# Kernel optimization log

Measured on AMD Instinct MI355X. Metric: run time of the kernel, lower is better.

## Reference

```python
import jax, jax.numpy as jnp
import numpy as np

N_SPATIAL = 65160
N_SPHERE = 2883
N_EDGES = 131072
D = 256             # latent_size
EDGE_IN_FIRST = 3 + 2 * D   # raw 3-dim displacements + sender + receiver = 515
EDGE_IN_REST = 3 * D        # after step 1 edges are D-dim = 768
NODE_IN = 2 * D
N_STEPS = 3


def _layernorm(x, g, b, eps=1e-5):
    m = jnp.mean(x, axis=-1, keepdims=True)
    v = jnp.var(x, axis=-1, keepdims=True)
    return (x - m) * jax.lax.rsqrt(v + eps) * g + b


def _mlp(x, W1, b1, g, o, W2, b2):
    # Linear -> relu -> LayerNorm -> Linear (matches hk.Sequential)
    h = jax.nn.relu(x @ W1 + b1)
    return _layernorm(h, g, o) @ W2 + b2


def setup_inputs() -> dict:
    key = jax.random.key(0)
    ks = jax.random.split(key, 12)

    def glorot(k, shape):
        return jax.random.normal(k, shape, jnp.float32) / np.sqrt(shape[0]).astype(np.float32)

    nodes = jax.random.normal(ks[0], (N_SPATIAL + N_SPHERE, D), jnp.float32)
    edges = jax.random.normal(ks[1], (N_EDGES, 3), jnp.float32)
    senders = jax.random.randint(ks[2], (N_EDGES,), 0, N_SPATIAL)
    # receivers index into the sphere portion of the concatenated node array
    receivers = jax.random.randint(ks[3], (N_EDGES,), 0, N_SPHERE) + N_SPATIAL
    return {
        "nodes": nodes,
        "edges": edges,
        "senders": senders,
        "receivers": receivers,
        "We1a": glorot(ks[4], (EDGE_IN_FIRST, D)),
        "We1b": glorot(ks[5], (EDGE_IN_REST, D)),
        "be1": jnp.zeros((D,), jnp.float32),
        "ge": jnp.ones((D,), jnp.float32),
        "oe": jnp.zeros((D,), jnp.float32),
        "We2": glorot(ks[6], (D, D)),
        "be2": jnp.zeros((D,), jnp.float32),
        "Wn1": glorot(ks[7], (NODE_IN, D)),
        "bn1": jnp.zeros((D,), jnp.float32),
        "gn": jnp.ones((D,), jnp.float32),
        "on": jnp.zeros((D,), jnp.float32),
        "Wn2": glorot(ks[8], (D, D)),
        "bn2": jnp.zeros((D,), jnp.float32),
        "n_spatial": N_SPATIAL,
        "n_sphere": N_SPHERE,
    }


def reference(nodes, edges, senders, receivers,
              We1a, We1b, be1, ge, oe, We2, be2,
              Wn1, bn1, gn, on, Wn2, bn2,
              n_spatial, n_sphere):
    recv_ids = receivers - n_spatial  # local sphere indices in [0, n_sphere)
    for step in range(N_STEPS):
        s = nodes[senders]                                   # [E, D]
        r = nodes[receivers]                                 # [E, D]
        edge_in = jnp.concatenate([edges, s, r], axis=1)     # [E, 3+2D] or [E, 3D]
        W1 = We1a if step == 0 else We1b
        edges = _mlp(edge_in, W1, be1, ge, oe, We2, be2)     # [E, D]
        messages = jax.ops.segment_sum(edges, recv_ids, num_segments=n_sphere)  # [S, D]
        sphere = nodes[n_spatial:]                           # [S, D]
        node_in = jnp.concatenate([sphere, messages], axis=1)
        updated = _mlp(node_in, Wn1, bn1, gn, on, Wn2, bn2)  # [S, D]
        nodes = jnp.concatenate([nodes[:n_spatial], updated], axis=0)
    return nodes[n_spatial:]
```

## Files before the change

### kernel.cpp

```cpp
#include <hip/hip_runtime.h>
#include <hip/hip_bf16.h>
#include <cstdint>
#include <cstddef>

#define N_SPATIAL_C 65160
#define N_SPHERE_C  2883
#define N_EDGES_C   131072

typedef short bf16x8 __attribute__((ext_vector_type(8)));
typedef float f32x4  __attribute__((ext_vector_type(4)));

__device__ inline float bf2f(ushort u) {
    union { uint u; float f; } c; c.u = ((uint)u) << 16; return c.f;
}
__device__ inline ushort f2bf(float f) {
    __hip_bfloat16 h = __float2bfloat16(f);
    union { __hip_bfloat16 h; ushort u; } c; c.h = h; return c.u;
}

#define VMWAIT8()  asm volatile("s_waitcnt vmcnt(8)" ::: "memory")
#define VMWAIT0()  asm volatile("s_waitcnt vmcnt(0)" ::: "memory")
#define LGKM0()    asm volatile("s_waitcnt lgkmcnt(0)" ::: "memory")
#define SBAR()     do { __builtin_amdgcn_sched_barrier(0); \
                        __builtin_amdgcn_s_barrier(); \
                        __builtin_amdgcn_sched_barrier(0); } while (0)

template<int EPI, int KI, int NBUF, typename OutT>
__global__ __launch_bounds__(256, 2) void mfma_gemm(
    const ushort* __restrict__ A, const ushort* __restrict__ Bt,
    OutT* __restrict__ C, int M, int lda, int ldc,
    const float* __restrict__ bias,
    const float* __restrict__ g, const float* __restrict__ o,
    const ushort* __restrict__ P, const int* __restrict__ senders,
    const float* __restrict__ Rf, const int* __restrict__ receivers,
    const int* __restrict__ cntv, const float* __restrict__ bxv)
{
    constexpr int CHR = KI / 8;
    __shared__ __align__(16) ushort lds[NBUF][64 * KI];

    const int nt = (M + 63) >> 6;
    if ((int)blockIdx.x >= nt) return;
    const int G    = gridDim.x;
    const int t    = threadIdx.x;
    const int w    = t >> 6;
    const int lane = t & 63;
    const int lo   = lane & 15, hi = lane >> 4, sw = lo & 7;
    const int bn   = w * 64;
    const int rl   = t >> 4, q = t & 15, c0 = q * 16;

    auto STAGE = [&](int buf, int tileIdx) {
#pragma unroll
        for (int i = 0; i < (64 * CHR) / 256; ++i) {
            int ci = i * 256 + t;
            int r  = ci / CHR;
            int cs = ci % CHR;
            int cg = cs ^ (r & 7);
            int rg = tileIdx * 64 + r; if (rg >= M) rg = M - 1;
            const ushort* gp = A + (size_t)rg * lda + cg * 8;
            const ushort* lp = &lds[buf][(size_t)(i * 256 + w * 64) * 8];
            __builtin_amdgcn_global_load_lds(
                (const __attribute__((address_space(1))) unsigned int*)gp,
                (__attribute__((address_space(3))) unsigned int*)lp, 16, 0, 0);
        }
    };

    bf16x8 breg[(NBUF == 2) ? 8 : 1][4];
    if constexpr (NBUF == 2) {
#pragma unroll
        for (int ks = 0; ks < 8; ++ks)
#pragma unroll
            for (int ct = 0; ct < 4; ++ct)
                breg[ks][ct] = *reinterpret_cast<const bf16x8*>(
                    Bt + (size_t)(bn + ct * 16 + lo) * KI + ks * 32 + hi * 8);
        STAGE(0, blockIdx.x);
    }

    int cur = 0;
    for (int tt = blockIdx.x; tt < nt; tt += G) {
        if constexpr (NBUF == 1) {
            STAGE(0, tt);
            VMWAIT0();
        } else {
            int tn = tt + G;
            if (tn < nt) { STAGE(cur ^ 1, tn); VMWAIT8(); }
            else         { VMWAIT0(); }
        }
        SBAR();

        const ushort* At = lds[cur];
        f32x4 acc[4][4];
#pragma unroll
        for (int rt = 0; rt < 4; ++rt)
#pragma unroll
            for (int ct = 0; ct < 4; ++ct)
#pragma unroll
                for (int j = 0; j < 4; ++j) acc[rt][ct][j] = 0.f;

#pragma unroll
        for (int ks = 0; ks < KI / 32; ++ks) {
            bf16x8 av[4], bv[4];
#pragma unroll
            for (int rt = 0; rt < 4; ++rt) {
                int row = rt * 16 + lo;
                av[rt] = *reinterpret_cast<const bf16x8*>(
                    At + ((size_t)row * CHR + ((ks * 4 + hi) ^ sw)) * 8);
            }
            if constexpr (NBUF == 2) {
#pragma unroll
                for (int ct = 0; ct < 4; ++ct) bv[ct] = breg[ks][ct];
            } else {
#pragma unroll
                for (int ct = 0; ct < 4; ++ct)
                    bv[ct] = *reinterpret_cast<const bf16x8*>(
                        Bt + (size_t)(bn + ct * 16 + lo) * KI + ks * 32 + hi * 8);
            }
#pragma unroll
            for (int rt = 0; rt < 4; ++rt)
#pragma unroll
                for (int ct = 0; ct < 4; ++ct)
                    acc[rt][ct] = __builtin_amdgcn_mfma_f32_16x16x32_bf16(
                        av[rt], bv[ct], acc[rt][ct], 0, 0, 0);
        }

        float* xbuf = (float*)lds[cur];
#pragma unroll
        for (int ph = 0; ph < 4; ++ph) {
            LGKM0(); SBAR();
#pragma unroll
            for (int ct = 0; ct < 4; ++ct)
#pragma unroll
                for (int reg = 0; reg < 4; ++reg)
                    xbuf[(size_t)(hi * 4 + reg) * 260 + (bn + ct * 16 + lo)] =
                        acc[ph][ct][reg];
            LGKM0(); SBAR();

            int rowg = tt * 64 + ph * 16 + rl;
            bool ok  = rowg < M;
            int rowc = ok ? rowg : M - 1;

            float x[16];
#pragma unroll
            for (int jj = 0; jj < 4; ++jj) {
                f32x4 v = *reinterpret_cast<const f32x4*>(
                    xbuf + (size_t)rl * 260 + c0 + jj * 4);
                x[jj*4+0] = v[0]; x[jj*4+1] = v[1];
                x[jj*4+2] = v[2]; x[jj*4+3] = v[3];
            }
            if (bias) {
#pragma unroll
                for (int jj = 0; jj < 4; ++jj) {
                    f32x4 v = *reinterpret_cast<const f32x4*>(bias + c0 + jj * 4);
                    x[jj*4+0] += v[0]; x[jj*4+1] += v[1];
                    x[jj*4+2] += v[2]; x[jj*4+3] += v[3];
                }
            }
            if (EPI == 1 && cntv) {
                float cf = (float)cntv[rowc];
#pragma unroll
                for (int jj = 0; jj < 4; ++jj) {
                    f32x4 v = *reinterpret_cast<const f32x4*>(bxv + c0 + jj * 4);
                    x[jj*4+0] += cf * v[0]; x[jj*4+1] += cf * v[1];
                    x[jj*4+2] += cf * v[2]; x[jj*4+3] += cf * v[3];
                }
            }
            if (EPI == 2) {
                int sIdx = senders[rowc];
                int rIdx = receivers[rowc] - N_SPATIAL_C;
                bf16x8 p0 = *reinterpret_cast<const bf16x8*>(P + (size_t)sIdx * 256 + c0);
                bf16x8 p1 = *reinterpret_cast<const bf16x8*>(P + (size_t)sIdx * 256 + c0 + 8);
#pragma unroll
                for (int j = 0; j < 8; ++j) {
                    x[j]     += bf2f((ushort)p0[j]);
                    x[8 + j] += bf2f((ushort)p1[j]);
                }
#pragma unroll
                for (int jj = 0; jj < 4; ++jj) {
                    f32x4 v = *reinterpret_cast<const f32x4*>(
                        Rf + (size_t)rIdx * 256 + c0 + jj * 4);
                    x[jj*4+0] += v[0]; x[jj*4+1] += v[1];
                    x[jj*4+2] += v[2]; x[jj*4+3] += v[3];
                }
            }
            if (EPI >= 1) {
#pragma unroll
                for (int j = 0; j < 16; ++j) x[j] = fmaxf(x[j], 0.f);
                float s1 = 0.f, s2 = 0.f;
#pragma unroll
                for (int j = 0; j < 16; ++j) { s1 += x[j]; s2 += x[j] * x[j]; }
#pragma unroll
                for (int m = 1; m < 16; m <<= 1) {
                    s1 += __shfl_xor(s1, m);
                    s2 += __shfl_xor(s2, m);
                }
                float mean = s1 * (1.f / 256.f);
                float var  = s2 * (1.f / 256.f) - mean * mean;
                float rstd = rsqrtf(var + 1e-5f);
#pragma unroll
                for (int jj = 0; jj < 4; ++jj) {
                    f32x4 gv = *reinterpret_cast<const f32x4*>(g + c0 + jj * 4);
                    f32x4 ov = *reinterpret_cast<const f32x4*>(o + c0 + jj * 4);
#pragma unroll
                    for (int e = 0; e < 4; ++e)
                        x[jj*4+e] = (x[jj*4+e] - mean) * rstd * gv[e] + ov[e];
                }
            }
            if (ok) {
                if constexpr (sizeof(OutT) == 2) {
                    bf16x8 s0, s1v;
#pragma unroll
                    for (int j = 0; j < 8; ++j) {
                        s0[j]  = (short)f2bf(x[j]);
                        s1v[j] = (short)f2bf(x[8 + j]);
                    }
                    ushort* Cp = (ushort*)C + (size_t)rowg * ldc + c0;
                    *reinterpret_cast<bf16x8*>(Cp)     = s0;
                    *reinterpret_cast<bf16x8*>(Cp + 8) = s1v;
                } else {
                    float* Cp = (float*)C + (size_t)rowg * ldc + c0;
#pragma unroll
                    for (int jj = 0; jj < 4; ++jj) {
                        f32x4 v;
                        v[0]=x[jj*4+0]; v[1]=x[jj*4+1];
                        v[2]=x[jj*4+2]; v[3]=x[jj*4+3];
                        *reinterpret_cast<f32x4*>(Cp + jj * 4) = v;
                    }
                }
            }
        }
        LGKM0(); SBAR();
        if constexpr (NBUF == 2) cur ^= 1;
    }
}

__global__ __launch_bounds__(256) void fuse0(
    const float* __restrict__ edges3, const float* __restrict__ Ae,
    const ushort* __restrict__ P, const int* __restrict__ senders,
    const float* __restrict__ Rf, const int* __restrict__ receivers,
    const float* __restrict__ be1, const float* __restrict__ g,
    const float* __restrict__ o, ushort* __restrict__ H)
{
    int row  = blockIdx.x * 4 + (threadIdx.x >> 6);
    int lane = threadIdx.x & 63;
    int c = lane * 4;

    float e0 = edges3[(size_t)row * 3 + 0];
    float e1 = edges3[(size_t)row * 3 + 1];
    float e2 = edges3[(size_t)row * 3 + 2];
    int s = senders[row];
    int r = receivers[row] - N_SPATIAL_C;
    ushort4 pv = *reinterpret_cast<const ushort4*>(P + (size_t)s * 256 + c);
    float4  rv = *reinterpret_cast<const float4*>(Rf + (size_t)r * 256 + c);

    float pw[4] = {bf2f(pv.x), bf2f(pv.y), bf2f(pv.z), bf2f(pv.w)};
    float rw[4] = {rv.x, rv.y, rv.z, rv.w};
    float x[4];
#pragma unroll
    for (int j = 0; j < 4; ++j) {
        x[j] = e0 * Ae[c + j] + e1 * Ae[256 + c + j] + e2 * Ae[512 + c + j]
             + be1[c + j] + pw[j] + rw[j];
        x[j] = fmaxf(x[j], 0.f);
    }
    float s1 = x[0] + x[1] + x[2] + x[3];
    float s2 = x[0]*x[0] + x[1]*x[1] + x[2]*x[2] + x[3]*x[3];
#pragma unroll
    for (int m = 32; m > 0; m >>= 1) { s1 += __shfl_xor(s1, m); s2 += __shfl_xor(s2, m); }
    float mean = s1 * (1.f / 256.f);
    float var  = s2 * (1.f / 256.f) - mean * mean;
    float rstd = rsqrtf(var + 1e-5f);
#pragma unroll
    for (int j = 0; j < 4; ++j) {
        float y = (x[j] - mean) * rstd * g[c + j] + o[c + j];
        H[(size_t)row * 256 + c + j] = f2bf(y);
    }
}

__global__ void count_k(const int* __restrict__ receivers, int* __restrict__ cnt)
{
    int e = blockIdx.x * 256 + threadIdx.x;
    if (e < N_EDGES_C) atomicAdd(&cnt[receivers[e] - N_SPATIAL_C], 1);
}

__global__ void scan_k(const int* __restrict__ cnt, int* __restrict__ row_start)
{
    __shared__ int sums[257];
    const int CH = 12;
    int t = threadIdx.x;
    int local = 0;
    for (int i = 0; i < CH; ++i) {
        int idx = t * CH + i;
        if (idx < N_SPHERE_C) local += cnt[idx];
    }
    sums[t] = local;
    __syncthreads();
    if (t == 0) {
        int run = 0;
        for (int i = 0; i < 256; ++i) { int v = sums[i]; sums[i] = run; run += v; }
        sums[256] = run;
    }
    __syncthreads();
    int base = sums[t];
    for (int i = 0; i < CH; ++i) {
        int idx = t * CH + i;
        if (idx < N_SPHERE_C) { row_start[idx] = base; base += cnt[idx]; }
    }
    if (t == 0) row_start[N_SPHERE_C] = sums[256];
}

__global__ void fill_k(const int* __restrict__ receivers, const int* __restrict__ row_start,
                       int* __restrict__ cursor, int* __restrict__ csr)
{
    int e = blockIdx.x * 256 + threadIdx.x;
    if (e < N_EDGES_C) {
        int rid = receivers[e] - N_SPATIAL_C;
        int pos = atomicAdd(&cursor[rid], 1);
        csr[row_start[rid] + pos] = e;
    }
}

__global__ __launch_bounds__(256) void seg_gather(
    const ushort* __restrict__ H, const int* __restrict__ row_start,
    const int* __restrict__ csr, ushort* __restrict__ S, int ldS)
{
    __shared__ float red[3][64][4];
    int n = blockIdx.x;
    int sub = threadIdx.x >> 6, l = threadIdx.x & 63, c = l * 4;
    int beg = row_start[n], end = row_start[n + 1];
    float a0 = 0.f, a1 = 0.f, a2 = 0.f, a3 = 0.f;
    for (int i = beg + sub; i < end; i += 4) {
        int e = csr[i];
        ushort4 v = *reinterpret_cast<const ushort4*>(H + (size_t)e * 256 + c);
        a0 += bf2f(v.x); a1 += bf2f(v.y); a2 += bf2f(v.z); a3 += bf2f(v.w);
    }
    if (sub) { red[sub-1][l][0]=a0; red[sub-1][l][1]=a1; red[sub-1][l][2]=a2; red[sub-1][l][3]=a3; }
    __syncthreads();
    if (sub == 0) {
#pragma unroll
        for (int s_ = 0; s_ < 3; ++s_) {
            a0 += red[s_][l][0]; a1 += red[s_][l][1];
            a2 += red[s_][l][2]; a3 += red[s_][l][3];
        }
        ushort4 u; u.x = f2bf(a0); u.y = f2bf(a1); u.z = f2bf(a2); u.w = f2bf(a3);
        *reinterpret_cast<ushort4*>(S + (size_t)n * ldS + c) = u;
    }
}

__global__ __launch_bounds__(256) void wprod_kernel(
    const float* __restrict__ We2, const float* __restrict__ Bsrc,
    ushort* __restrict__ Wt, int ldd, int koff)
{
    __shared__ float colB[256];
    int j = blockIdx.x, k = threadIdx.x;
    colB[k] = Bsrc[(size_t)k * 256 + j];
    __syncthreads();
    const float* wrow = We2 + (size_t)k * 256;
    float acc = 0.f;
    for (int t = 0; t < 256; ++t) acc += wrow[t] * colB[t];
    Wt[(size_t)j * ldd + koff + k] = f2bf(acc);
}

__global__ void bvecprod_kernel(const float* __restrict__ base, const float* __restrict__ bvec,
                                const float* __restrict__ W, float* __restrict__ bout)
{
    int j = threadIdx.x;
    float acc = base ? base[j] : 0.f;
    for (int k = 0; k < 256; ++k) acc += bvec[k] * W[(size_t)k * 256 + j];
    bout[j] = acc;
}

__global__ void tcast2(const float* __restrict__ W, ushort* __restrict__ Wt, int ldd)
{
    __shared__ float tbuf[16][17];
    int k0 = blockIdx.x * 16, n0 = blockIdx.y * 16;
    int tx = threadIdx.x, ty = threadIdx.y;
    tbuf[ty][tx] = W[(size_t)(k0 + ty) * 256 + n0 + tx];
    __syncthreads();
    Wt[(size_t)(n0 + ty) * ldd + k0 + tx] = f2bf(tbuf[tx][ty]);
}

__global__ void cast_f32_bf16(const float* __restrict__ src, ushort* __restrict__ dst, int n4)
{
    int i = blockIdx.x * 256 + threadIdx.x;
    if (i < n4) {
        float4 v = *reinterpret_cast<const float4*>(src + (size_t)i * 4);
        ushort4 u;
        u.x = f2bf(v.x); u.y = f2bf(v.y); u.z = f2bf(v.z); u.w = f2bf(v.w);
        *reinterpret_cast<ushort4*>(dst + (size_t)i * 4) = u;
    }
}

__global__ void cast_sphere(const float* __restrict__ nodes, ushort* __restrict__ node_in)
{
    int n = blockIdx.x, d = threadIdx.x;
    node_in[(size_t)n * 512 + d] =
        f2bf(nodes[(size_t)(N_SPATIAL_C + n) * 256 + d]);
}

extern "C" void kernel_launch(void* const* d_in, const int* in_sizes, int n_in,
                              void* d_out, int out_size, void* d_ws, size_t ws_size,
                              hipStream_t stream)
{
    const float* nodes     = (const float*)d_in[0];
    const float* edges3    = (const float*)d_in[1];
    const int*   senders   = (const int*)d_in[2];
    const int*   receivers = (const int*)d_in[3];
    const float* We1a      = (const float*)d_in[4];
    const float* We1b      = (const float*)d_in[5];
    const float* be1       = (const float*)d_in[6];
    const float* ge        = (const float*)d_in[7];
    const float* oe        = (const float*)d_in[8];
    const float* We2       = (const float*)d_in[9];
    const float* be2       = (const float*)d_in[10];
    const float* Wn1       = (const float*)d_in[11];
    const float* bn1       = (const float*)d_in[12];
    const float* gn        = (const float*)d_in[13];
    const float* on_       = (const float*)d_in[14];
    const float* Wn2       = (const float*)d_in[15];
    const float* bn2       = (const float*)d_in[16];

    const float* Ae  = We1a;
    const float* As_ = We1a + 3 * 256;
    const float* Ar  = We1a + 259 * 256;
    const float* Be  = We1b;
    const float* Bs_ = We1b + 256 * 256;
    const float* Br  = We1b + 512 * 256;
    const float* Wn1bot = Wn1 + 256 * 256;

    char* ws = (char*)d_ws;
    size_t off = 0;
    auto alloc = [&](size_t b) -> char* {
        char* p = ws + off;
        off += (b + 255) & ~(size_t)255;
        return p;
    };
    ushort* H          = (ushort*)alloc((size_t)N_EDGES_C * 256 * 2);
    ushort* Pb         = (ushort*)alloc((size_t)N_SPATIAL_C * 256 * 2);
    ushort* nodes_bf   = (ushort*)alloc((size_t)N_SPATIAL_C * 256 * 2);
    float*  Rf         = (float*)alloc((size_t)N_SPHERE_C * 256 * 4);
    ushort* node_in_bf = (ushort*)alloc((size_t)N_SPHERE_C * 512 * 2);
    ushort* nH         = (ushort*)alloc((size_t)N_SPHERE_C * 256 * 2);
    ushort* Ast  = (ushort*)alloc(256 * 256 * 2);
    ushort* Art  = (ushort*)alloc(256 * 256 * 2);
    ushort* Bst  = (ushort*)alloc(256 * 256 * 2);
    ushort* Brt  = (ushort*)alloc(256 * 256 * 2);
    ushort* Wn2t = (ushort*)alloc(256 * 256 * 2);
    ushort* Wft  = (ushort*)alloc(256 * 256 * 2);
    ushort* Bnt  = (ushort*)alloc(256 * 512 * 2);
    float*  bfc  = (float*)alloc(256 * 4);
    float*  bxv  = (float*)alloc(256 * 4);
    int* cnt       = (int*)alloc(N_SPHERE_C * 4);
    int* cursor    = (int*)alloc(N_SPHERE_C * 4);
    int* row_start = (int*)alloc((N_SPHERE_C + 1) * 4);
    int* csr       = (int*)alloc((size_t)N_EDGES_C * 4);

    hipMemsetAsync(cnt, 0, N_SPHERE_C * 4, stream);
    hipMemsetAsync(cursor, 0, N_SPHERE_C * 4, stream);
    count_k<<<(N_EDGES_C + 255) / 256, 256, 0, stream>>>(receivers, cnt);
    scan_k<<<1, 256, 0, stream>>>(cnt, row_start);
    fill_k<<<(N_EDGES_C + 255) / 256, 256, 0, stream>>>(receivers, row_start, cursor, csr);

    dim3 tb(16, 16);
    tcast2<<<dim3(16, 16), tb, 0, stream>>>(As_, Ast, 256);
    tcast2<<<dim3(16, 16), tb, 0, stream>>>(Ar,  Art, 256);
    tcast2<<<dim3(16, 16), tb, 0, stream>>>(Bs_, Bst, 256);
    tcast2<<<dim3(16, 16), tb, 0, stream>>>(Br,  Brt, 256);
    tcast2<<<dim3(16, 16), tb, 0, stream>>>(Wn2, Wn2t, 256);
    tcast2<<<dim3(16, 16), tb, 0, stream>>>(Wn1, Bnt, 512);
    wprod_kernel<<<256, 256, 0, stream>>>(We2, Be, Wft, 256, 0);
    wprod_kernel<<<256, 256, 0, stream>>>(We2, Wn1bot, Bnt, 512, 256);
    bvecprod_kernel<<<1, 256, 0, stream>>>(be1, be2, Be, bfc);
    bvecprod_kernel<<<1, 256, 0, stream>>>(nullptr, be2, Wn1bot, bxv);

    cast_f32_bf16<<<(N_SPATIAL_C * 64 + 255) / 256, 256, 0, stream>>>(
        nodes, nodes_bf, N_SPATIAL_C * 64);
    cast_sphere<<<N_SPHERE_C, 256, 0, stream>>>(nodes, node_in_bf);

    const int GBIG = 512;
    const int GS = (N_SPHERE_C + 63) / 64;

    const float* nul = nullptr;

    mfma_gemm<0, 256, 2, ushort><<<GBIG, 256, 0, stream>>>(
        nodes_bf, Ast, Pb, N_SPATIAL_C, 256, 256,
        nul, nul, nul, nullptr, nullptr, nul, nullptr, nullptr, nul);

    for (int step = 0; step < 3; ++step) {
        mfma_gemm<0, 256, 2, float><<<GS, 256, 0, stream>>>(
            node_in_bf, step == 0 ? Art : Brt, Rf, N_SPHERE_C, 512, 256,
            nul, nul, nul, nullptr, nullptr, nul, nullptr, nullptr, nul);

        if (step == 0) {
            fuse0<<<N_EDGES_C / 4, 256, 0, stream>>>(
                edges3, Ae, Pb, senders, Rf, receivers, be1, ge, oe, H);
            mfma_gemm<0, 256, 2, ushort><<<GBIG, 256, 0, stream>>>(
                nodes_bf, Bst, Pb, N_SPATIAL_C, 256, 256,
                nul, nul, nul, nullptr, nullptr, nul, nullptr, nullptr, nul);
        } else {
            mfma_gemm<2, 256, 2, ushort><<<GBIG, 256, 0, stream>>>(
                H, Wft, H, N_EDGES_C, 256, 256,
                bfc, ge, oe, Pb, senders, Rf, receivers, nullptr, nul);
        }

        seg_gather<<<N_SPHERE_C, 256, 0, stream>>>(H, row_start, csr,
                                                   node_in_bf + 256, 512);

        mfma_gemm<1, 512, 1, ushort><<<GS, 256, 0, stream>>>(
            node_in_bf, Bnt, nH, N_SPHERE_C, 512, 256,
            bn1, gn, on_, nullptr, nullptr, nul, nullptr, cnt, bxv);

        if (step < 2) {
            mfma_gemm<0, 256, 2, ushort><<<GS, 256, 0, stream>>>(
                nH, Wn2t, node_in_bf, N_SPHERE_C, 256, 512,
                bn2, nul, nul, nullptr, nullptr, nul, nullptr, nullptr, nul);
        } else {
            mfma_gemm<0, 256, 2, float><<<GS, 256, 0, stream>>>(
                nH, Wn2t, (float*)d_out, N_SPHERE_C, 256, 256,
                bn2, nul, nul, nullptr, nullptr, nul, nullptr, nullptr, nul);
        }
    }
}
```

Before: 665.9 us.

## Replace LDS-staged persistent GEMM with direct-load register GEMM and register epilogue

Rewrites the MFMA GEMM kernel. It drops the persistent grid with double-buffered LDS staging through global_load_lds and swizzling. Each block now handles one 64-row tile, and A and B fragments are read straight from global memory into registers. The operand order is swapped so each lane holds a row's columns, which lets the bias, gather-add, ReLU and LayerNorm epilogue run in registers with only a small LDS cross-wave reduction, instead of transposing through LDS. This removes LDS traffic and barriers and raises the occupancy target, at the cost of uncoalesced, unreused global A and B loads with no prefetch overlap.

```diff
diff --git a/kernel.cpp b/kernel.cpp
--- a/kernel.cpp
+++ b/kernel.cpp
@@ -18,15 +18,8 @@
     union { __hip_bfloat16 h; ushort u; } c; c.h = h; return c.u;
 }
 
-#define VMWAIT8()  asm volatile("s_waitcnt vmcnt(8)" ::: "memory")
-#define VMWAIT0()  asm volatile("s_waitcnt vmcnt(0)" ::: "memory")
-#define LGKM0()    asm volatile("s_waitcnt lgkmcnt(0)" ::: "memory")
-#define SBAR()     do { __builtin_amdgcn_sched_barrier(0); \
-                        __builtin_amdgcn_s_barrier(); \
-                        __builtin_amdgcn_sched_barrier(0); } while (0)
-
-template<int EPI, int KI, int NBUF, typename OutT>
-__global__ __launch_bounds__(256, 2) void mfma_gemm(
+template<int EPI, int KI, typename OutT>
+__global__ __launch_bounds__(256, 3) void mfma_gemm(
     const ushort* __restrict__ A, const ushort* __restrict__ Bt,
     OutT* __restrict__ C, int M, int lda, int ldc,
     const float* __restrict__ bias,
@@ -35,200 +28,162 @@
     const float* __restrict__ Rf, const int* __restrict__ receivers,
     const int* __restrict__ cntv, const float* __restrict__ bxv)
 {
-    constexpr int CHR = KI / 8;
-    __shared__ __align__(16) ushort lds[NBUF][64 * KI];
-
-    const int nt = (M + 63) >> 6;
-    if ((int)blockIdx.x >= nt) return;
-    const int G    = gridDim.x;
+    __shared__ float red1[4][64];
+    __shared__ float red2[4][64];
+
+    const int m0   = blockIdx.x * 64;
     const int t    = threadIdx.x;
     const int w    = t >> 6;
     const int lane = t & 63;
-    const int lo   = lane & 15, hi = lane >> 4, sw = lo & 7;
+    const int lo   = lane & 15, hi = lane >> 4;
     const int bn   = w * 64;
-    const int rl   = t >> 4, q = t & 15, c0 = q * 16;
-
-    auto STAGE = [&](int buf, int tileIdx) {
-#pragma unroll
-        for (int i = 0; i < (64 * CHR) / 256; ++i) {
-            int ci = i * 256 + t;
-            int r  = ci / CHR;
-            int cs = ci % CHR;
-            int cg = cs ^ (r & 7);
-            int rg = tileIdx * 64 + r; if (rg >= M) rg = M - 1;
-            const ushort* gp = A + (size_t)rg * lda + cg * 8;
-            const ushort* lp = &lds[buf][(size_t)(i * 256 + w * 64) * 8];
-            __builtin_amdgcn_global_load_lds(
-                (const __attribute__((address_space(1))) unsigned int*)gp,
-                (__attribute__((address_space(3))) unsigned int*)lp, 16, 0, 0);
-        }
-    };
-
-    bf16x8 breg[(NBUF == 2) ? 8 : 1][4];
-    if constexpr (NBUF == 2) {
-#pragma unroll
-        for (int ks = 0; ks < 8; ++ks)
+
+    f32x4 acc[4][4];
+#pragma unroll
+    for (int rt = 0; rt < 4; ++rt)
+#pragma unroll
+        for (int ct = 0; ct < 4; ++ct)
+#pragma unroll
+            for (int j = 0; j < 4; ++j) acc[rt][ct][j] = 0.f;
+
+    int arow[4];
+#pragma unroll
+    for (int rt = 0; rt < 4; ++rt) {
+        int r = m0 + rt * 16 + lo;
+        arow[rt] = (r < M) ? r : (M - 1);
+    }
+
+#pragma unroll
+    for (int ks = 0; ks < KI / 32; ++ks) {
+        bf16x8 bt[4], ar[4];
+#pragma unroll
+        for (int ct = 0; ct < 4; ++ct)
+            bt[ct] = *reinterpret_cast<const bf16x8*>(
+                Bt + (size_t)(bn + ct * 16 + lo) * KI + ks * 32 + hi * 8);
+#pragma unroll
+        for (int rt = 0; rt < 4; ++rt)
+            ar[rt] = *reinterpret_cast<const bf16x8*>(
+                A + (size_t)arow[rt] * lda + ks * 32 + hi * 8);
+#pragma unroll
+        for (int rt = 0; rt < 4; ++rt)
 #pragma unroll
             for (int ct = 0; ct < 4; ++ct)
-                breg[ks][ct] = *reinterpret_cast<const bf16x8*>(
-                    Bt + (size_t)(bn + ct * 16 + lo) * KI + ks * 32 + hi * 8);
-        STAGE(0, blockIdx.x);
-    }
-
-    int cur = 0;
-    for (int tt = blockIdx.x; tt < nt; tt += G) {
-        if constexpr (NBUF == 1) {
-            STAGE(0, tt);
-            VMWAIT0();
-        } else {
-            int tn = tt + G;
-            if (tn < nt) { STAGE(cur ^ 1, tn); VMWAIT8(); }
-            else         { VMWAIT0(); }
-        }
-        SBAR();
-
-        const ushort* At = lds[cur];
-        f32x4 acc[4][4];
-#pragma unroll
-        for (int rt = 0; rt < 4; ++rt)
+                acc[rt][ct] = __builtin_amdgcn_mfma_f32_16x16x32_bf16(
+                    bt[ct], ar[rt], acc[rt][ct], 0, 0, 0);
+    }
+
+    const int c00 = bn + hi * 4;
+
+#pragma unroll
+    for (int rt = 0; rt < 4; ++rt) {
+        int e  = m0 + rt * 16 + lo;
+        int ec = (e < M) ? e : (M - 1);
+
+        if (bias) {
+#pragma unroll
+            for (int ct = 0; ct < 4; ++ct) {
+                f32x4 v = *reinterpret_cast<const f32x4*>(bias + c00 + ct * 16);
+#pragma unroll
+                for (int j = 0; j < 4; ++j) acc[rt][ct][j] += v[j];
+            }
+        }
+        if (EPI == 1 && cntv) {
+            float cf = (float)cntv[ec];
+#pragma unroll
+            for (int ct = 0; ct < 4; ++ct) {
+                f32x4 v = *reinterpret_cast<const f32x4*>(bxv + c00 + ct * 16);
+#pragma unroll
+                for (int j = 0; j < 4; ++j) acc[rt][ct][j] += cf * v[j];
+            }
+        }
+        if (EPI == 2) {
+            int sIdx = senders[ec];
+            int rIdx = receivers[ec] - N_SPATIAL_C;
+#pragma unroll
+            for (int ct = 0; ct < 4; ++ct) {
+                ushort4 pv = *reinterpret_cast<const ushort4*>(
+                    P + (size_t)sIdx * 256 + c00 + ct * 16);
+                f32x4 rv = *reinterpret_cast<const f32x4*>(
+                    Rf + (size_t)rIdx * 256 + c00 + ct * 16);
+                acc[rt][ct][0] += bf2f(pv.x) + rv[0];
+                acc[rt][ct][1] += bf2f(pv.y) + rv[1];
+                acc[rt][ct][2] += bf2f(pv.z) + rv[2];
+                acc[rt][ct][3] += bf2f(pv.w) + rv[3];
+            }
+        }
+        if (EPI >= 1) {
 #pragma unroll
             for (int ct = 0; ct < 4; ++ct)
 #pragma unroll
-                for (int j = 0; j < 4; ++j) acc[rt][ct][j] = 0.f;
-
-#pragma unroll
-        for (int ks = 0; ks < KI / 32; ++ks) {
-            bf16x8 av[4], bv[4];
+                for (int j = 0; j < 4; ++j)
+                    acc[rt][ct][j] = fmaxf(acc[rt][ct][j], 0.f);
+        }
+    }
+
+    if (EPI >= 1) {
+        float s1v[4], s2v[4];
+#pragma unroll
+        for (int rt = 0; rt < 4; ++rt) {
+            float s1 = 0.f, s2 = 0.f;
+#pragma unroll
+            for (int ct = 0; ct < 4; ++ct)
+#pragma unroll
+                for (int j = 0; j < 4; ++j) {
+                    float y = acc[rt][ct][j];
+                    s1 += y; s2 += y * y;
+                }
+            s1 += __shfl_xor(s1, 16); s2 += __shfl_xor(s2, 16);
+            s1 += __shfl_xor(s1, 32); s2 += __shfl_xor(s2, 32);
+            s1v[rt] = s1; s2v[rt] = s2;
+        }
+        if (hi == 0) {
 #pragma unroll
             for (int rt = 0; rt < 4; ++rt) {
-                int row = rt * 16 + lo;
-                av[rt] = *reinterpret_cast<const bf16x8*>(
-                    At + ((size_t)row * CHR + ((ks * 4 + hi) ^ sw)) * 8);
-            }
-            if constexpr (NBUF == 2) {
-#pragma unroll
-                for (int ct = 0; ct < 4; ++ct) bv[ct] = breg[ks][ct];
+                red1[w][rt * 16 + lo] = s1v[rt];
+                red2[w][rt * 16 + lo] = s2v[rt];
+            }
+        }
+        __syncthreads();
+
+#pragma unroll
+        for (int rt = 0; rt < 4; ++rt) {
+            int el = rt * 16 + lo;
+            float t1 = red1[0][el] + red1[1][el] + red1[2][el] + red1[3][el];
+            float t2 = red2[0][el] + red2[1][el] + red2[2][el] + red2[3][el];
+            float mean = t1 * (1.f / 256.f);
+            float var  = t2 * (1.f / 256.f) - mean * mean;
+            float rstd = rsqrtf(var + 1e-5f);
+#pragma unroll
+            for (int ct = 0; ct < 4; ++ct) {
+                f32x4 gv = *reinterpret_cast<const f32x4*>(g + c00 + ct * 16);
+                f32x4 ov = *reinterpret_cast<const f32x4*>(o + c00 + ct * 16);
+#pragma unroll
+                for (int j = 0; j < 4; ++j)
+                    acc[rt][ct][j] = (acc[rt][ct][j] - mean) * rstd * gv[j] + ov[j];
+            }
+        }
+    }
+
+#pragma unroll
+    for (int rt = 0; rt < 4; ++rt) {
+        int e = m0 + rt * 16 + lo;
+        if (e < M) {
+            if constexpr (sizeof(OutT) == 2) {
+#pragma unroll
+                for (int ct = 0; ct < 4; ++ct) {
+                    ushort4 u;
+                    u.x = f2bf(acc[rt][ct][0]); u.y = f2bf(acc[rt][ct][1]);
+                    u.z = f2bf(acc[rt][ct][2]); u.w = f2bf(acc[rt][ct][3]);
+                    *reinterpret_cast<ushort4*>(
+                        (ushort*)C + (size_t)e * ldc + c00 + ct * 16) = u;
+                }
             } else {
 #pragma unroll
                 for (int ct = 0; ct < 4; ++ct)
-                    bv[ct] = *reinterpret_cast<const bf16x8*>(
-                        Bt + (size_t)(bn + ct * 16 + lo) * KI + ks * 32 + hi * 8);
-            }
-#pragma unroll
-            for (int rt = 0; rt < 4; ++rt)
-#pragma unroll
-                for (int ct = 0; ct < 4; ++ct)
-                    acc[rt][ct] = __builtin_amdgcn_mfma_f32_16x16x32_bf16(
-                        av[rt], bv[ct], acc[rt][ct], 0, 0, 0);
-        }
-
-        float* xbuf = (float*)lds[cur];
-#pragma unroll
-        for (int ph = 0; ph < 4; ++ph) {
-            LGKM0(); SBAR();
-#pragma unroll
-            for (int ct = 0; ct < 4; ++ct)
-#pragma unroll
-                for (int reg = 0; reg < 4; ++reg)
-                    xbuf[(size_t)(hi * 4 + reg) * 260 + (bn + ct * 16 + lo)] =
-                        acc[ph][ct][reg];
-            LGKM0(); SBAR();
-
-            int rowg = tt * 64 + ph * 16 + rl;
-            bool ok  = rowg < M;
-            int rowc = ok ? rowg : M - 1;
-
-            float x[16];
-#pragma unroll
-            for (int jj = 0; jj < 4; ++jj) {
-                f32x4 v = *reinterpret_cast<const f32x4*>(
-                    xbuf + (size_t)rl * 260 + c0 + jj * 4);
-                x[jj*4+0] = v[0]; x[jj*4+1] = v[1];
-                x[jj*4+2] = v[2]; x[jj*4+3] = v[3];
-            }
-            if (bias) {
-#pragma unroll
-                for (int jj = 0; jj < 4; ++jj) {
-                    f32x4 v = *reinterpret_cast<const f32x4*>(bias + c0 + jj * 4);
-                    x[jj*4+0] += v[0]; x[jj*4+1] += v[1];
-                    x[jj*4+2] += v[2]; x[jj*4+3] += v[3];
-                }
-            }
-            if (EPI == 1 && cntv) {
-                float cf = (float)cntv[rowc];
-#pragma unroll
-                for (int jj = 0; jj < 4; ++jj) {
-                    f32x4 v = *reinterpret_cast<const f32x4*>(bxv + c0 + jj * 4);
-                    x[jj*4+0] += cf * v[0]; x[jj*4+1] += cf * v[1];
-                    x[jj*4+2] += cf * v[2]; x[jj*4+3] += cf * v[3];
-                }
-            }
-            if (EPI == 2) {
-                int sIdx = senders[rowc];
-                int rIdx = receivers[rowc] - N_SPATIAL_C;
-                bf16x8 p0 = *reinterpret_cast<const bf16x8*>(P + (size_t)sIdx * 256 + c0);
-                bf16x8 p1 = *reinterpret_cast<const bf16x8*>(P + (size_t)sIdx * 256 + c0 + 8);
-#pragma unroll
-                for (int j = 0; j < 8; ++j) {
-                    x[j]     += bf2f((ushort)p0[j]);
-                    x[8 + j] += bf2f((ushort)p1[j]);
-                }
-#pragma unroll
-                for (int jj = 0; jj < 4; ++jj) {
-                    f32x4 v = *reinterpret_cast<const f32x4*>(
-                        Rf + (size_t)rIdx * 256 + c0 + jj * 4);
-                    x[jj*4+0] += v[0]; x[jj*4+1] += v[1];
-                    x[jj*4+2] += v[2]; x[jj*4+3] += v[3];
-                }
-            }
-            if (EPI >= 1) {
-#pragma unroll
-                for (int j = 0; j < 16; ++j) x[j] = fmaxf(x[j], 0.f);
-                float s1 = 0.f, s2 = 0.f;
-#pragma unroll
-                for (int j = 0; j < 16; ++j) { s1 += x[j]; s2 += x[j] * x[j]; }
-#pragma unroll
-                for (int m = 1; m < 16; m <<= 1) {
-                    s1 += __shfl_xor(s1, m);
-                    s2 += __shfl_xor(s2, m);
-                }
-                float mean = s1 * (1.f / 256.f);
-                float var  = s2 * (1.f / 256.f) - mean * mean;
-                float rstd = rsqrtf(var + 1e-5f);
-#pragma unroll
-                for (int jj = 0; jj < 4; ++jj) {
-                    f32x4 gv = *reinterpret_cast<const f32x4*>(g + c0 + jj * 4);
-                    f32x4 ov = *reinterpret_cast<const f32x4*>(o + c0 + jj * 4);
-#pragma unroll
-                    for (int e = 0; e < 4; ++e)
-                        x[jj*4+e] = (x[jj*4+e] - mean) * rstd * gv[e] + ov[e];
-                }
-            }
-            if (ok) {
-                if constexpr (sizeof(OutT) == 2) {
-                    bf16x8 s0, s1v;
-#pragma unroll
-                    for (int j = 0; j < 8; ++j) {
-                        s0[j]  = (short)f2bf(x[j]);
-                        s1v[j] = (short)f2bf(x[8 + j]);
-                    }
-                    ushort* Cp = (ushort*)C + (size_t)rowg * ldc + c0;
-                    *reinterpret_cast<bf16x8*>(Cp)     = s0;
-                    *reinterpret_cast<bf16x8*>(Cp + 8) = s1v;
-                } else {
-                    float* Cp = (float*)C + (size_t)rowg * ldc + c0;
-#pragma unroll
-                    for (int jj = 0; jj < 4; ++jj) {
-                        f32x4 v;
-                        v[0]=x[jj*4+0]; v[1]=x[jj*4+1];
-                        v[2]=x[jj*4+2]; v[3]=x[jj*4+3];
-                        *reinterpret_cast<f32x4*>(Cp + jj * 4) = v;
-                    }
-                }
-            }
-        }
-        LGKM0(); SBAR();
-        if constexpr (NBUF == 2) cur ^= 1;
+                    *reinterpret_cast<f32x4*>(
+                        (float*)C + (size_t)e * ldc + c00 + ct * 16) = acc[rt][ct];
+            }
+        }
     }
 }
 
@@ -474,28 +429,28 @@
         nodes, nodes_bf, N_SPATIAL_C * 64);
     cast_sphere<<<N_SPHERE_C, 256, 0, stream>>>(nodes, node_in_bf);
 
-    const int GBIG = 512;
+    const int GE = N_EDGES_C / 64;
+    const int GP = (N_SPATIAL_C + 63) / 64;
     const int GS = (N_SPHERE_C + 63) / 64;
-
     const float* nul = nullptr;
 
-    mfma_gemm<0, 256, 2, ushort><<<GBIG, 256, 0, stream>>>(
+    mfma_gemm<0, 256, ushort><<<GP, 256, 0, stream>>>(
         nodes_bf, Ast, Pb, N_SPATIAL_C, 256, 256,
         nul, nul, nul, nullptr, nullptr, nul, nullptr, nullptr, nul);
 
     for (int step = 0; step < 3; ++step) {
-        mfma_gemm<0, 256, 2, float><<<GS, 256, 0, stream>>>(
+        mfma_gemm<0, 256, float><<<GS, 256, 0, stream>>>(
             node_in_bf, step == 0 ? Art : Brt, Rf, N_SPHERE_C, 512, 256,
             nul, nul, nul, nullptr, nullptr, nul, nullptr, nullptr, nul);
 
         if (step == 0) {
             fuse0<<<N_EDGES_C / 4, 256, 0, stream>>>(
                 edges3, Ae, Pb, senders, Rf, receivers, be1, ge, oe, H);
-            mfma_gemm<0, 256, 2, ushort><<<GBIG, 256, 0, stream>>>(
+            mfma_gemm<0, 256, ushort><<<GP, 256, 0, stream>>>(
                 nodes_bf, Bst, Pb, N_SPATIAL_C, 256, 256,
                 nul, nul, nul, nullptr, nullptr, nul, nullptr, nullptr, nul);
         } else {
-            mfma_gemm<2, 256, 2, ushort><<<GBIG, 256, 0, stream>>>(
+            mfma_gemm<2, 256, ushort><<<GE, 256, 0, stream>>>(
                 H, Wft, H, N_EDGES_C, 256, 256,
                 bfc, ge, oe, Pb, senders, Rf, receivers, nullptr, nul);
         }
@@ -503,16 +458,16 @@
         seg_gather<<<N_SPHERE_C, 256, 0, stream>>>(H, row_start, csr,
                                                    node_in_bf + 256, 512);
 
-        mfma_gemm<1, 512, 1, ushort><<<GS, 256, 0, stream>>>(
+        mfma_gemm<1, 512, ushort><<<GS, 256, 0, stream>>>(
             node_in_bf, Bnt, nH, N_SPHERE_C, 512, 256,
             bn1, gn, on_, nullptr, nullptr, nul, nullptr, cnt, bxv);
 
         if (step < 2) {
-            mfma_gemm<0, 256, 2, ushort><<<GS, 256, 0, stream>>>(
+            mfma_gemm<0, 256, ushort><<<GS, 256, 0, stream>>>(
                 nH, Wn2t, node_in_bf, N_SPHERE_C, 256, 512,
                 bn2, nul, nul, nullptr, nullptr, nul, nullptr, nullptr, nul);
         } else {
-            mfma_gemm<0, 256, 2, float><<<GS, 256, 0, stream>>>(
+            mfma_gemm<0, 256, float><<<GS, 256, 0, stream>>>(
                 nH, Wn2t, (float*)d_out, N_SPHERE_C, 256, 256,
                 bn2, nul, nul, nullptr, nullptr, nul, nullptr, nullptr, nul);
         }
```

After: 751.5 us. 1.13x slower.
